# Kernel tuning notes

Measured on AMD Instinct MI355X. Metric: run time of the kernel, lower is better.

Reference implementation:

```python
import jax, jax.numpy as jnp
import numpy as np

NUM_GAUSS = 64
MAX_R = 5.0
ANG_TO_NM = 0.1  # du.ANG_TO_NM_SCALE
L = 4
C_NODE = 256
C_HID = 256
MAX_ATOMS = 100
B = 512      # building blocks
NPB = 32     # atoms per block
K = 20       # max_neighbors
N = B * NPB
E = N * K
GAUSS_COEFF = -0.5 / (MAX_R / (NUM_GAUSS - 1)) ** 2


def setup_inputs() -> dict:
    rng = np.random.default_rng(0)
    # all atoms of a block inside a 2.5A cube -> every pair within MAX_R=5A,
    # so radius_graph capped at K neighbors == K-nearest graph (fixed E).
    pos = (rng.random((B, NPB, 3)) * 2.5).astype(np.float32)
    d = np.linalg.norm(pos[:, :, None, :] - pos[:, None, :, :], axis=-1)  # [B,n,n]
    ii = np.arange(NPB)
    d[:, ii, ii] = np.inf  # loop=False
    nbr = np.argsort(d, axis=-1)[:, :, :K]  # [B,n,K] nearest neighbors
    base = (np.arange(B) * NPB)[:, None, None]
    row = np.broadcast_to(ii[None, :, None], (B, NPB, K)) + base
    col = nbr + base
    edge_index = np.stack([row.reshape(-1), col.reshape(-1)]).astype(np.int64)

    key = jax.random.key(0)
    ks = jax.random.split(key, 8)

    def lin(k, fi, fo):
        return jax.random.normal(k, (L, fi, fo), jnp.float32) / np.sqrt(fi).astype(np.float32)

    d_e_in = 2 * C_NODE + 1 + NUM_GAUSS  # 577
    return {
        'local_coords': jnp.asarray(pos.reshape(N, 3)),
        'atom_types': jax.random.randint(ks[0], (N,), 1, MAX_ATOMS + 1),  # 1..max_atoms
        'edge_index': jnp.asarray(edge_index),
        'batch_bb': jnp.repeat(jnp.arange(B, dtype=jnp.int32), NPB),
        'atom_embed': jax.random.normal(ks[1], (MAX_ATOMS, C_NODE), jnp.float32) * 0.1,
        'offset': jnp.linspace(0.0, MAX_R, NUM_GAUSS, dtype=jnp.float32),
        'We1': lin(ks[2], d_e_in, C_HID), 'be1': jnp.zeros((L, C_HID), jnp.float32),
        'We2': lin(ks[3], C_HID, C_HID), 'be2': jnp.zeros((L, C_HID), jnp.float32),
        'Wn1': lin(ks[4], C_HID + C_NODE, C_HID), 'bn1': jnp.zeros((L, C_HID), jnp.float32),
        'Wn2': lin(ks[5], C_HID, C_NODE), 'bn2': jnp.zeros((L, C_NODE), jnp.float32),
    }


def _forward(local_coords, atom_types, edge_index, batch_bb, atom_embed, offset,
             We1, be1, We2, be2, Wn1, bn1, Wn2, bn2):
    row, col = edge_index[0], edge_index[1]
    h = atom_embed[atom_types - 1]                      # [N, C_NODE]
    # Gaussian smearing of pairwise distances (Angstrom)
    dvec = local_coords[col] - local_coords[row]        # [E, 3]
    dist = jnp.sqrt(jnp.sum(dvec * dvec, axis=-1))      # [E]
    edge_attr = jnp.exp(GAUSS_COEFF * (dist[:, None] - offset[None, :]) ** 2)  # [E, 64]
    coord = local_coords * ANG_TO_NM
    cdiff = coord[row] - coord[col]
    radial = jnp.sum(cdiff * cdiff, axis=-1, keepdims=True)  # [E, 1]
    nblocks = batch_bb.shape[0] // NPB  # static
    for l in range(L):  # small fixed layer count
        e_in = jnp.concatenate([h[row], h[col], radial, edge_attr], axis=-1)  # [E, 577]
        m = jax.nn.relu(e_in @ We1[l] + be1[l])
        m = jax.nn.relu(m @ We2[l] + be2[l])                 # edge_mlp output [E, C_HID]
        agg = jax.ops.segment_sum(m, row, num_segments=N)    # scatter-sum to nodes
        n_in = jnp.concatenate([h, agg], axis=-1)            # [N, C_NODE + C_HID]
        out = jax.nn.relu(n_in @ Wn1[l] + bn1[l]) @ Wn2[l] + bn2[l]
        node_update = h + out                                # residual inside E_GCL
        h = h + node_update                                  # outer residual in forward
    # global_mean_pool over building blocks
    s = jax.ops.segment_sum(h, batch_bb, num_segments=B)
    cnt = jax.ops.segment_sum(jnp.ones((h.shape[0], 1), h.dtype), batch_bb, num_segments=B)
    return s / cnt


def reference(local_coords, atom_types, edge_index, batch_bb, atom_embed, offset,
              We1, be1, We2, be2, Wn1, bn1, Wn2, bn2):
    return _forward(local_coords, atom_types, edge_index, batch_bb, atom_embed, offset,
                    We1, be1, We2, be2, Wn1, bn1, Wn2, bn2)
```

## Files before the change

kernel.cpp:

```cpp
#include <hip/hip_runtime.h>
#include <hip/hip_bf16.h>
#include <stdint.h>

#define NATOMS 16384
#define ETOT   327680
#define NLAYER 4

typedef __hip_bfloat16 bf16;
using bf16x8 = __attribute__((ext_vector_type(8))) short;
using bf16x4 = __attribute__((ext_vector_type(4))) short;
using f32x4  = __attribute__((ext_vector_type(4))) float;

#define LDSF_STRIDE 260

__device__ __forceinline__ float bf2f(short s) {
  union { float f; unsigned u; } x; x.u = ((unsigned)(unsigned short)s) << 16; return x.f;
}
__device__ __forceinline__ short f2bf(float f) {
  bf16 b = __float2bfloat16(f);
  return *(short*)&b;
}

__device__ __forceinline__ void async16(const void* g, void* l) {
  __builtin_amdgcn_global_load_lds(
      (const __attribute__((address_space(1))) unsigned int*)g,
      (__attribute__((address_space(3))) unsigned int*)l, 16, 0, 0);
}

template<int KTOT, int EPI, int MT>
__global__ void __launch_bounds__(256, 2)
gemm_k(const bf16* A, const bf16* A2, const bf16* B,
       bf16* Obf, int ldOut, const float* bias,
       float* Hf, bf16* Hbf)
{
  __shared__ __align__(16) char smem[49152];
  __shared__ float s_bias[256];

  const int tid  = threadIdx.x;
  const int w    = tid >> 6;
  const int lane = tid & 63;
  const int q    = lane >> 4;
  const int t16  = lane & 15;
  const size_t row0 = (size_t)blockIdx.x * MT;
  const int ncol0 = blockIdx.y * 256;
  constexpr int MI = MT / 16;
  constexpr int AI = MT / 32;

  if constexpr (EPI == 2 || EPI == 4) s_bias[tid] = bias[tid];

  f32x4 acc[MI][4] = {};

  constexpr int NCHUNK = KTOT / 64;
  for (int kc = 0; kc < NCHUNK; ++kc) {
    const int k0 = kc * 64;
    const bf16* Asrc; int k0e; int ldA;
    if constexpr (KTOT == 512) {
      if (k0 < 256) { Asrc = A;  k0e = k0;       }
      else          { Asrc = A2; k0e = k0 - 256; }
      ldA = 256;
    } else {
      Asrc = A; k0e = k0; ldA = KTOT;
    }

    __syncthreads();
    #pragma unroll
    for (int ii = 0; ii < AI; ++ii) {
      int i = w * AI + ii;
      int f = i * 64 + lane;
      int m = f >> 3, s = f & 7;
      int ko = s ^ (m & 7);
      const bf16* g = Asrc + (row0 + (size_t)m) * ldA + (size_t)(k0e + ko * 8);
      async16(g, smem + i * 1024);
    }
    #pragma unroll
    for (int ii = 0; ii < 8; ++ii) {
      int i = w * 8 + ii;
      int f = i * 64 + lane;
      int n = f >> 3, s = f & 7;
      int ko = s ^ (n & 7);
      const bf16* g = B + (size_t)(ncol0 + n) * KTOT + (size_t)(k0 + ko * 8);
      async16(g, smem + 16384 + i * 1024);
    }
    __syncthreads();

    #pragma unroll
    for (int ks = 0; ks < 2; ++ks) {
      bf16x8 av[MI]; bf16x8 bv[4];
      const int ko = q + 4 * ks;
      #pragma unroll
      for (int mi = 0; mi < MI; ++mi) {
        int m = 16 * mi + t16;
        int f = m * 8 + (ko ^ (m & 7));
        av[mi] = *(const bf16x8*)(smem + f * 16);
      }
      #pragma unroll
      for (int ni = 0; ni < 4; ++ni) {
        int n = 64 * w + 16 * ni + t16;
        int f = n * 8 + (ko ^ (n & 7));
        bv[ni] = *(const bf16x8*)(smem + 16384 + f * 16);
      }
      #pragma unroll
      for (int mi = 0; mi < MI; ++mi)
        #pragma unroll
        for (int ni = 0; ni < 4; ++ni)
          acc[mi][ni] = __builtin_amdgcn_mfma_f32_16x16x32_bf16(
              av[mi], bv[ni], acc[mi][ni], 0, 0, 0);
    }
  }

  float* lds_f = (float*)smem;
  #pragma unroll
  for (int mi = 0; mi < MI; ++mi) {
    __syncthreads();
    #pragma unroll
    for (int ni = 0; ni < 4; ++ni)
      #pragma unroll
      for (int r = 0; r < 4; ++r)
        lds_f[(4 * q + r) * LDSF_STRIDE + 64 * w + 16 * ni + t16] = acc[mi][ni][r];
    __syncthreads();
    #pragma unroll
    for (int j = 0; j < 2; ++j) {
      int task = tid + 256 * j;
      int rr = task >> 5, cg = task & 31;
      int c0 = cg * 8;
      size_t rg = row0 + 16 * mi + rr;
      f32x4 v0 = *(const f32x4*)(lds_f + rr * LDSF_STRIDE + c0);
      f32x4 v1 = *(const f32x4*)(lds_f + rr * LDSF_STRIDE + c0 + 4);
      float v[8] = {v0[0], v0[1], v0[2], v0[3], v1[0], v1[1], v1[2], v1[3]};
      if constexpr (EPI == 0) {
        bf16x8 o;
        #pragma unroll
        for (int k = 0; k < 8; ++k) o[k] = f2bf(v[k]);
        *(bf16x8*)(Obf + rg * ldOut + (ncol0 + c0)) = o;
      } else if constexpr (EPI == 2) {
        bf16x8 o;
        #pragma unroll
        for (int k = 0; k < 8; ++k) o[k] = f2bf(fmaxf(v[k] + s_bias[c0 + k], 0.f));
        *(bf16x8*)(Obf + rg * 256 + c0) = o;
      } else {
        f32x4 h0 = *(const f32x4*)(Hf + rg * 256 + c0);
        f32x4 h1 = *(const f32x4*)(Hf + rg * 256 + c0 + 4);
        float hh[8] = {h0[0], h0[1], h0[2], h0[3], h1[0], h1[1], h1[2], h1[3]};
        bf16x8 o; f32x4 n0, n1;
        #pragma unroll
        for (int k = 0; k < 8; ++k) {
          float hn = 2.f * hh[k] + v[k] + s_bias[c0 + k];
          o[k] = f2bf(hn);
          if (k < 4) n0[k] = hn; else n1[k - 4] = hn;
        }
        *(f32x4*)(Hf + rg * 256 + c0)     = n0;
        *(f32x4*)(Hf + rg * 256 + c0 + 4) = n1;
        *(bf16x8*)(Hbf + rg * 256 + c0) = o;
      }
    }
  }
}

#define BBPITCH 1040
#define M1O     33280
#define METAO   74240

__global__ void __launch_bounds__(256, 2)
bb_edge_fused(const bf16* WgT_l, const bf16* We2T_l, const float* off,
              const float* pos, const int* eidx, const bf16* Prc,
              const float* be1, const float* wrad, const float* be2, bf16* Agg)
{
  __shared__ __align__(16) char smem[75776];
  int*   s_rc   = (int*)  (smem + METAO);
  float* s_rad  = (float*)(smem + METAO + 320);
  float* s_dist = (float*)(smem + METAO + 640);
  float* s_off  = (float*)(smem + METAO + 960);

  const int tid  = threadIdx.x;
  const int w    = tid >> 6;
  const int lane = tid & 63;
  const int q    = lane >> 4;
  const int t16  = lane & 15;
  const int bb   = blockIdx.x;
  const int node0 = bb * 32;
  const int ebase = bb * 640;

  float b1r[4][4], wrr[4][4];
  #pragma unroll
  for (int fi = 0; fi < 4; ++fi) {
    int fb = 64 * w + 16 * fi + 4 * q;
    f32x4 tb = *(const f32x4*)(be1 + fb);
    f32x4 tw = *(const f32x4*)(wrad + fb);
    #pragma unroll
    for (int r = 0; r < 4; ++r) { b1r[fi][r] = tb[r]; wrr[fi][r] = tw[r]; }
  }
  float b2v[4];
  #pragma unroll
  for (int ni = 0; ni < 4; ++ni) b2v[ni] = be2[64 * w + 16 * ni + t16];

  bf16x8 wgf[4][2];
  #pragma unroll
  for (int fi = 0; fi < 4; ++fi)
    #pragma unroll
    for (int ks = 0; ks < 2; ++ks) {
      int feat = 64 * w + 16 * fi + t16;
      int ko = q + 4 * ks;
      wgf[fi][ks] = *(const bf16x8*)(WgT_l + (size_t)feat * 64 + ko * 8);
    }

  if (tid < 64) s_off[tid] = off[tid];

  {
    int row = tid >> 3, seg = tid & 7;
    const bf16* src = Prc + (size_t)(node0 + row) * 512 + seg * 64;
    char* dst = smem + row * BBPITCH + seg * 128;
    #pragma unroll
    for (int j = 0; j < 8; ++j)
      *(bf16x8*)(dst + j * 16) = *(const bf16x8*)(src + j * 8);
  }

  const float GC = -0.5f / ((5.0f / 63.0f) * (5.0f / 63.0f));

  for (int c = 0; c < 8; ++c) {
    __syncthreads();
    if (tid < 80) {
      int e = ebase + c * 80 + tid;
      int r = eidx[e], cc = eidx[ETOT + e];
      float dx = pos[cc * 3 + 0] - pos[r * 3 + 0];
      float dy = pos[cc * 3 + 1] - pos[r * 3 + 1];
      float dz = pos[cc * 3 + 2] - pos[r * 3 + 2];
      float d2 = dx * dx + dy * dy + dz * dz;
      float d = sqrtf(d2);
      s_rc[tid]  = (r & 31) | ((cc & 31) << 8);
      s_rad[tid] = 0.01f * d2;
      s_dist[tid] = d;
      #pragma unroll
      for (int oct = 0; oct < 8; ++oct) {
        bf16x8 v;
        #pragma unroll
        for (int j = 0; j < 8; ++j) {
          float t = d - s_off[oct * 8 + j];
          v[j] = f2bf(__expf(GC * t * t));
        }
        int f = tid * 8 + (oct ^ (tid & 7));
        *(bf16x8*)(smem + M1O + f * 16) = v;
      }
    }
    __syncthreads();

    f32x4 acc1[4][5] = {};
    #pragma unroll
    for (int ks = 0; ks < 2; ++ks) {
      const int ko = q + 4 * ks;
      bf16x8 gv[5];
      #pragma unroll
      for (int ci = 0; ci < 5; ++ci) {
        int e = 16 * ci + t16;
        int f = e * 8 + (ko ^ (e & 7));
        gv[ci] = *(const bf16x8*)(smem + M1O + f * 16);
      }
      #pragma unroll
      for (int fi = 0; fi < 4; ++fi)
        #pragma unroll
        for (int ci = 0; ci < 5; ++ci)
          acc1[fi][ci] = __builtin_amdgcn_mfma_f32_16x16x32_bf16(
              wgf[fi][ks], gv[ci], acc1[fi][ci], 0, 0, 0);
    }
    __syncthreads();

    #pragma unroll
    for (int ci = 0; ci < 5; ++ci) {
      int e = 16 * ci + t16;
      int rc = s_rc[e];
      int rl = rc & 31, cl = (rc >> 8) & 31;
      float rad = s_rad[e];
      #pragma unroll
      for (int fi = 0; fi < 4; ++fi) {
        int fb = 64 * w + 16 * fi + 4 * q;
        bf16x4 pr = *(const bf16x4*)(smem + rl * BBPITCH + fb * 2);
        bf16x4 pc = *(const bf16x4*)(smem + cl * BBPITCH + 512 + fb * 2);
        bf16x4 o;
        #pragma unroll
        for (int r = 0; r < 4; ++r) {
          float val = acc1[fi][ci][r] + b1r[fi][r] + rad * wrr[fi][r]
                    + bf2f(pr[r]) + bf2f(pc[r]);
          o[r] = f2bf(fmaxf(val, 0.f));
        }
        int u = (16 * w + 4 * fi + q) ^ (e & 14);
        *(bf16x4*)(smem + M1O + e * 512 + u * 8) = o;
      }
    }
    __syncthreads();

    f32x4 acc2[5][4] = {};
    #pragma unroll
    for (int kc = 0; kc < 4; ++kc) {
      bf16x8 bv[4][2];
      #pragma unroll
      for (int ni = 0; ni < 4; ++ni)
        #pragma unroll
        for (int ks = 0; ks < 2; ++ks) {
          int n = 64 * w + 16 * ni + t16;
          int ko = q + 4 * ks;
          bv[ni][ks] = *(const bf16x8*)(We2T_l + (size_t)n * 256 + kc * 64 + ko * 8);
        }
      #pragma unroll
      for (int ks = 0; ks < 2; ++ks) {
        const int ko = q + 4 * ks;
        bf16x8 av[5];
        #pragma unroll
        for (int mi = 0; mi < 5; ++mi) {
          int e = 16 * mi + t16;
          int ub = (2 * (8 * kc + ko)) ^ (t16 & 14);
          av[mi] = *(const bf16x8*)(smem + M1O + e * 512 + ub * 8);
        }
        #pragma unroll
        for (int mi = 0; mi < 5; ++mi)
          #pragma unroll
          for (int ni = 0; ni < 4; ++ni)
            acc2[mi][ni] = __builtin_amdgcn_mfma_f32_16x16x32_bf16(
                av[mi], bv[ni][ks], acc2[mi][ni], 0, 0, 0);
      }
    }

    #pragma unroll
    for (int ni = 0; ni < 4; ++ni) {
      float b = b2v[ni];
      float pp[5];
      #pragma unroll
      for (int mi = 0; mi < 5; ++mi) {
        float s = 0.f;
        #pragma unroll
        for (int r = 0; r < 4; ++r) s += fmaxf(acc2[mi][ni][r] + b, 0.f);
        pp[mi] = s;
      }
      #pragma unroll
      for (int nn = 0; nn < 4; ++nn) {
        float s = 0.f;
        #pragma unroll
        for (int mi = 0; mi < 5; ++mi) {
          int g = 4 * mi + q;
          if (g >= 5 * nn && g <= 5 * nn + 4) s += pp[mi];
        }
        s += __shfl_xor(s, 16, 64);
        s += __shfl_xor(s, 32, 64);
        if (q == nn)
          Agg[(size_t)(node0 + c * 4 + nn) * 256 + 64 * w + 16 * ni + t16] =
              __float2bfloat16(s);
      }
    }
  }
}

__global__ void wrct_kernel(const float* We1, bf16* WrcT) {
  int idx = blockIdx.x * 256 + threadIdx.x;
  int k = idx & 255, np = (idx >> 8) & 511, l = idx >> 17;
  float v = (np < 256)
      ? We1[((size_t)l * 577 + k) * 256 + np]
      : We1[((size_t)l * 577 + 256 + k) * 256 + (np - 256)];
  WrcT[idx] = __float2bfloat16(v);
}
__global__ void wgt_kernel(const float* We1, bf16* WgT) {
  int idx = blockIdx.x * 256 + threadIdx.x;
  int k = idx & 63, n = (idx >> 6) & 255, l = idx >> 14;
  WgT[idx] = __float2bfloat16(We1[((size_t)l * 577 + 513 + k) * 256 + n]);
}
__global__ void wrad_kernel(const float* We1, float* wrad) {
  int idx = blockIdx.x * 256 + threadIdx.x;
  int n = idx & 255, l = idx >> 8;
  wrad[idx] = We1[((size_t)l * 577 + 512) * 256 + n];
}
__global__ void trans_kernel(const float* src, bf16* dst, int R, int C) {
  int idx = blockIdx.x * 256 + threadIdx.x;
  int k = idx % R, rest = idx / R;
  int n = rest % C, l = rest / C;
  dst[idx] = __float2bfloat16(src[((size_t)l * R + k) * C + n]);
}

__global__ void h0_kernel(const int* types, const float* emb, float* h, bf16* hbf) {
  int i = blockIdx.x, c = threadIdx.x;
  float v = emb[(size_t)(types[i] - 1) * 256 + c];
  h[(size_t)i * 256 + c] = v;
  hbf[(size_t)i * 256 + c] = __float2bfloat16(v);
}

__global__ void pool_kernel(const float* h, float* out) {
  int b = blockIdx.x, c = threadIdx.x;
  float s = 0.f;
  #pragma unroll
  for (int j = 0; j < 32; ++j) s += h[((size_t)b * 32 + j) * 256 + c];
  out[(size_t)b * 256 + c] = s * (1.0f / 32.0f);
}

extern "C" void kernel_launch(void* const* d_in, const int* in_sizes, int n_in,
                              void* d_out, int out_size, void* d_ws, size_t ws_size,
                              hipStream_t stream) {
  const float* pos   = (const float*)d_in[0];
  const int*   atype = (const int*)  d_in[1];
  const int*   eidx  = (const int*)  d_in[2];
  const float* emb   = (const float*)d_in[4];
  const float* off   = (const float*)d_in[5];
  const float* We1   = (const float*)d_in[6];
  const float* be1   = (const float*)d_in[7];
  const float* We2   = (const float*)d_in[8];
  const float* be2   = (const float*)d_in[9];
  const float* Wn1   = (const float*)d_in[10];
  const float* bn1   = (const float*)d_in[11];
  const float* Wn2   = (const float*)d_in[12];
  const float* bn2   = (const float*)d_in[13];
  float* out = (float*)d_out;

  size_t o = 0;
  auto carve = [&](size_t bytes) {
    void* p = (char*)d_ws + o;
    o += (bytes + 255) & ~(size_t)255;
    return p;
  };
  float* h     = (float*)carve((size_t)NATOMS * 256 * 4);
  bf16*  hbf   = (bf16*) carve((size_t)NATOMS * 256 * 2);
  bf16*  Prc   = (bf16*) carve((size_t)NATOMS * 512 * 2);
  bf16*  aggbf = (bf16*) carve((size_t)NATOMS * 256 * 2);
  bf16*  WrcT  = (bf16*) carve((size_t)NLAYER * 512 * 256 * 2);
  bf16*  WgT   = (bf16*) carve((size_t)NLAYER * 256 * 64 * 2);
  bf16*  We2T  = (bf16*) carve((size_t)NLAYER * 256 * 256 * 2);
  bf16*  Wn1T  = (bf16*) carve((size_t)NLAYER * 256 * 512 * 2);
  bf16*  Wn2T  = (bf16*) carve((size_t)NLAYER * 256 * 256 * 2);
  float* wradp = (float*)carve((size_t)NLAYER * 256 * 4);

  wrct_kernel<<<2048, 256, 0, stream>>>(We1, WrcT);
  wgt_kernel <<< 256, 256, 0, stream>>>(We1, WgT);
  wrad_kernel<<<   4, 256, 0, stream>>>(We1, wradp);
  trans_kernel<<<1024, 256, 0, stream>>>(We2, We2T, 256, 256);
  trans_kernel<<<2048, 256, 0, stream>>>(Wn1, Wn1T, 512, 256);
  trans_kernel<<<1024, 256, 0, stream>>>(Wn2, Wn2T, 256, 256);
  h0_kernel  <<<NATOMS, 256, 0, stream>>>(atype, emb, h, hbf);

  for (int l = 0; l < NLAYER; ++l) {
    gemm_k<256, 0, 64><<<dim3(256, 2), 256, 0, stream>>>(
        hbf, nullptr, WrcT + (size_t)l * 512 * 256, Prc, 512, nullptr,
        nullptr, nullptr);
    bb_edge_fused<<<512, 256, 0, stream>>>(
        WgT + (size_t)l * 256 * 64, We2T + (size_t)l * 256 * 256, off, pos,
        eidx, Prc, be1 + l * 256, wradp + l * 256, be2 + l * 256, aggbf);
    gemm_k<512, 2, 64><<<dim3(256, 1), 256, 0, stream>>>(
        hbf, aggbf, Wn1T + (size_t)l * 256 * 512, aggbf, 256, bn1 + l * 256,
        nullptr, nullptr);
    gemm_k<256, 4, 64><<<dim3(256, 1), 256, 0, stream>>>(
        aggbf, nullptr, Wn2T + (size_t)l * 256 * 256, nullptr, 0, bn2 + l * 256,
        h, hbf);
  }

  pool_kernel<<<512, 256, 0, stream>>>(h, out);
}
```

Baseline: 710.3 us.

## Compute Gaussian features in registers and precompute edge metadata once per block

Edge metadata (local row/col indices and scaled squared distance) for all 640 edges is now computed once before the chunk loop instead of per chunk by only 80 threads. Gaussian smearing is computed directly in registers in MFMA operand layout by every lane, which removes the shared-memory round trip and two barriers per chunk. Half of the We2 weights are kept in registers across chunks and the other half are loaded early to hide latency, while bias and radial weights move into LDS to free registers. This raises register pressure and LDS size, which could hurt occupancy at two blocks per CU, and recomputes exp values redundantly across waves.

Result: slower. 883.4 us (+24.4%).

```diff
diff --git a/kernel.cpp b/kernel.cpp
--- a/kernel.cpp
+++ b/kernel.cpp
@@ -158,18 +158,21 @@
 
 #define BBPITCH 1040
 #define M1O     33280
-#define METAO   74240
+#define RCO     74240
+#define RADO    75520
+#define B1O     78080
+#define WRO     79104
 
 __global__ void __launch_bounds__(256, 2)
 bb_edge_fused(const bf16* WgT_l, const bf16* We2T_l, const float* off,
               const float* pos, const int* eidx, const bf16* Prc,
               const float* be1, const float* wrad, const float* be2, bf16* Agg)
 {
-  __shared__ __align__(16) char smem[75776];
-  int*   s_rc   = (int*)  (smem + METAO);
-  float* s_rad  = (float*)(smem + METAO + 320);
-  float* s_dist = (float*)(smem + METAO + 640);
-  float* s_off  = (float*)(smem + METAO + 960);
+  __shared__ __align__(16) char smem[80128];
+  unsigned short* s_rc  = (unsigned short*)(smem + RCO);
+  float*          s_rad = (float*)(smem + RADO);
+  float*          s_b1  = (float*)(smem + B1O);
+  float*          s_wr  = (float*)(smem + WRO);
 
   const int tid  = threadIdx.x;
   const int w    = tid >> 6;
@@ -180,30 +183,29 @@
   const int node0 = bb * 32;
   const int ebase = bb * 640;
 
-  float b1r[4][4], wrr[4][4];
+  float offk[2][8];
   #pragma unroll
-  for (int fi = 0; fi < 4; ++fi) {
-    int fb = 64 * w + 16 * fi + 4 * q;
-    f32x4 tb = *(const f32x4*)(be1 + fb);
-    f32x4 tw = *(const f32x4*)(wrad + fb);
-    #pragma unroll
-    for (int r = 0; r < 4; ++r) { b1r[fi][r] = tb[r]; wrr[fi][r] = tw[r]; }
+  for (int ks = 0; ks < 2; ++ks) {
+    f32x4 o0 = *(const f32x4*)(off + (q + 4 * ks) * 8);
+    f32x4 o1 = *(const f32x4*)(off + (q + 4 * ks) * 8 + 4);
+    #pragma unroll
+    for (int j = 0; j < 4; ++j) { offk[ks][j] = o0[j]; offk[ks][4 + j] = o1[j]; }
   }
   float b2v[4];
   #pragma unroll
   for (int ni = 0; ni < 4; ++ni) b2v[ni] = be2[64 * w + 16 * ni + t16];
 
-  bf16x8 wgf[4][2];
+  bf16x8 bvp[2][4][2];
   #pragma unroll
-  for (int fi = 0; fi < 4; ++fi)
-    #pragma unroll
-    for (int ks = 0; ks < 2; ++ks) {
-      int feat = 64 * w + 16 * fi + t16;
-      int ko = q + 4 * ks;
-      wgf[fi][ks] = *(const bf16x8*)(WgT_l + (size_t)feat * 64 + ko * 8);
-    }
-
-  if (tid < 64) s_off[tid] = off[tid];
+  for (int kc = 0; kc < 2; ++kc)
+    #pragma unroll
+    for (int ni = 0; ni < 4; ++ni)
+      #pragma unroll
+      for (int ks = 0; ks < 2; ++ks) {
+        int n = 64 * w + 16 * ni + t16;
+        bvp[kc][ni][ks] =
+            *(const bf16x8*)(We2T_l + (size_t)n * 256 + kc * 64 + (q + 4 * ks) * 8);
+      }
 
   {
     int row = tid >> 3, seg = tid & 7;
@@ -213,71 +215,84 @@
     for (int j = 0; j < 8; ++j)
       *(bf16x8*)(dst + j * 16) = *(const bf16x8*)(src + j * 8);
   }
+  for (int i = tid; i < 640; i += 256) {
+    int e = ebase + i;
+    int r = eidx[e], cc = eidx[ETOT + e];
+    float dx = pos[cc * 3 + 0] - pos[r * 3 + 0];
+    float dy = pos[cc * 3 + 1] - pos[r * 3 + 1];
+    float dz = pos[cc * 3 + 2] - pos[r * 3 + 2];
+    float d2 = dx * dx + dy * dy + dz * dz;
+    s_rc[i]  = (unsigned short)((r & 31) | ((cc & 31) << 8));
+    s_rad[i] = 0.01f * d2;
+  }
+  s_b1[tid] = be1[tid];
+  s_wr[tid] = wrad[tid];
+  __syncthreads();
 
   const float GC = -0.5f / ((5.0f / 63.0f) * (5.0f / 63.0f));
 
   for (int c = 0; c < 8; ++c) {
-    __syncthreads();
-    if (tid < 80) {
-      int e = ebase + c * 80 + tid;
-      int r = eidx[e], cc = eidx[ETOT + e];
-      float dx = pos[cc * 3 + 0] - pos[r * 3 + 0];
-      float dy = pos[cc * 3 + 1] - pos[r * 3 + 1];
-      float dz = pos[cc * 3 + 2] - pos[r * 3 + 2];
-      float d2 = dx * dx + dy * dy + dz * dz;
-      float d = sqrtf(d2);
-      s_rc[tid]  = (r & 31) | ((cc & 31) << 8);
-      s_rad[tid] = 0.01f * d2;
-      s_dist[tid] = d;
-      #pragma unroll
-      for (int oct = 0; oct < 8; ++oct) {
-        bf16x8 v;
+    bf16x8 wgf[4][2];
+    #pragma unroll
+    for (int fi = 0; fi < 4; ++fi)
+      #pragma unroll
+      for (int ks = 0; ks < 2; ++ks) {
+        int feat = 64 * w + 16 * fi + t16;
+        wgf[fi][ks] = *(const bf16x8*)(WgT_l + (size_t)feat * 64 + (q + 4 * ks) * 8);
+      }
+
+    f32x4 acc[5][4] = {};
+    #pragma unroll
+    for (int ci = 0; ci < 5; ++ci) {
+      int eg = 80 * c + 16 * ci + t16;
+      float d = 10.f * sqrtf(s_rad[eg]);
+      bf16x8 gv[2];
+      #pragma unroll
+      for (int ks = 0; ks < 2; ++ks)
         #pragma unroll
         for (int j = 0; j < 8; ++j) {
-          float t = d - s_off[oct * 8 + j];
-          v[j] = f2bf(__expf(GC * t * t));
-        }
-        int f = tid * 8 + (oct ^ (tid & 7));
-        *(bf16x8*)(smem + M1O + f * 16) = v;
-      }
-    }
-    __syncthreads();
-
-    f32x4 acc1[4][5] = {};
-    #pragma unroll
-    for (int ks = 0; ks < 2; ++ks) {
-      const int ko = q + 4 * ks;
-      bf16x8 gv[5];
-      #pragma unroll
-      for (int ci = 0; ci < 5; ++ci) {
-        int e = 16 * ci + t16;
-        int f = e * 8 + (ko ^ (e & 7));
-        gv[ci] = *(const bf16x8*)(smem + M1O + f * 16);
-      }
-      #pragma unroll
-      for (int fi = 0; fi < 4; ++fi)
-        #pragma unroll
-        for (int ci = 0; ci < 5; ++ci)
-          acc1[fi][ci] = __builtin_amdgcn_mfma_f32_16x16x32_bf16(
-              wgf[fi][ks], gv[ci], acc1[fi][ci], 0, 0, 0);
-    }
-    __syncthreads();
-
+          float t = d - offk[ks][j];
+          gv[ks][j] = f2bf(__expf(GC * t * t));
+        }
+      #pragma unroll
+      for (int ks = 0; ks < 2; ++ks)
+        #pragma unroll
+        for (int fi = 0; fi < 4; ++fi)
+          acc[ci][fi] = __builtin_amdgcn_mfma_f32_16x16x32_bf16(
+              wgf[fi][ks], gv[ks], acc[ci][fi], 0, 0, 0);
+    }
+
+    bf16x8 bvl[2][4][2];
+    #pragma unroll
+    for (int kc = 0; kc < 2; ++kc)
+      #pragma unroll
+      for (int ni = 0; ni < 4; ++ni)
+        #pragma unroll
+        for (int ks = 0; ks < 2; ++ks) {
+          int n = 64 * w + 16 * ni + t16;
+          bvl[kc][ni][ks] = *(const bf16x8*)(We2T_l + (size_t)n * 256 +
+                                             (kc + 2) * 64 + (q + 4 * ks) * 8);
+        }
+
+    __syncthreads();
     #pragma unroll
     for (int ci = 0; ci < 5; ++ci) {
       int e = 16 * ci + t16;
-      int rc = s_rc[e];
+      int eg = 80 * c + e;
+      int rc = s_rc[eg];
       int rl = rc & 31, cl = (rc >> 8) & 31;
-      float rad = s_rad[e];
+      float rad = s_rad[eg];
       #pragma unroll
       for (int fi = 0; fi < 4; ++fi) {
         int fb = 64 * w + 16 * fi + 4 * q;
+        f32x4 tb = *(const f32x4*)(s_b1 + fb);
+        f32x4 tw = *(const f32x4*)(s_wr + fb);
         bf16x4 pr = *(const bf16x4*)(smem + rl * BBPITCH + fb * 2);
         bf16x4 pc = *(const bf16x4*)(smem + cl * BBPITCH + 512 + fb * 2);
         bf16x4 o;
         #pragma unroll
         for (int r = 0; r < 4; ++r) {
-          float val = acc1[fi][ci][r] + b1r[fi][r] + rad * wrr[fi][r]
+          float val = acc[ci][fi][r] + tb[r] + rad * tw[r]
                     + bf2f(pr[r]) + bf2f(pc[r]);
           o[r] = f2bf(fmaxf(val, 0.f));
         }
@@ -287,18 +302,13 @@
     }
     __syncthreads();
 
-    f32x4 acc2[5][4] = {};
+    #pragma unroll
+    for (int ci = 0; ci < 5; ++ci)
+      #pragma unroll
+      for (int ni = 0; ni < 4; ++ni)
+        acc[ci][ni] = f32x4{0.f, 0.f, 0.f, 0.f};
     #pragma unroll
     for (int kc = 0; kc < 4; ++kc) {
-      bf16x8 bv[4][2];
-      #pragma unroll
-      for (int ni = 0; ni < 4; ++ni)
-        #pragma unroll
-        for (int ks = 0; ks < 2; ++ks) {
-          int n = 64 * w + 16 * ni + t16;
-          int ko = q + 4 * ks;
-          bv[ni][ks] = *(const bf16x8*)(We2T_l + (size_t)n * 256 + kc * 64 + ko * 8);
-        }
       #pragma unroll
       for (int ks = 0; ks < 2; ++ks) {
         const int ko = q + 4 * ks;
@@ -313,8 +323,10 @@
         for (int mi = 0; mi < 5; ++mi)
           #pragma unroll
           for (int ni = 0; ni < 4; ++ni)
-            acc2[mi][ni] = __builtin_amdgcn_mfma_f32_16x16x32_bf16(
-                av[mi], bv[ni][ks], acc2[mi][ni], 0, 0, 0);
+            acc[mi][ni] = __builtin_amdgcn_mfma_f32_16x16x32_bf16(
+                av[mi],
+                (kc < 2) ? bvp[kc][ni][ks] : bvl[kc - 2][ni][ks],
+                acc[mi][ni], 0, 0, 0);
       }
     }
 
@@ -326,7 +338,7 @@
       for (int mi = 0; mi < 5; ++mi) {
         float s = 0.f;
         #pragma unroll
-        for (int r = 0; r < 4; ++r) s += fmaxf(acc2[mi][ni][r] + b, 0.f);
+        for (int r = 0; r < 4; ++r) s += fmaxf(acc[mi][ni][r] + b, 0.f);
         pp[mi] = s;
       }
       #pragma unroll
```
